# Performance work log

Measured on AMD Instinct MI355X. Metric: run time of the kernel, lower is better.

Reference implementation:

```python
import jax, jax.numpy as jnp
import numpy as np

B, C, H, W = 32, 256, 64, 64
HID = 16  # max(8, 256 // 16)


def setup_inputs() -> dict:
    key = jax.random.key(0)
    k1, k2, k3 = jax.random.split(key, 3)
    x = jax.random.normal(k1, (B, C, H, W), dtype=jnp.float32)
    # 1x1 conv weights (kernel spatial dims squeezed away)
    w1 = jax.random.normal(k2, (HID, C), dtype=jnp.float32) * (1.0 / np.sqrt(C))
    b1 = jnp.zeros((HID,), dtype=jnp.float32)
    w2 = jax.random.normal(k3, (C, HID), dtype=jnp.float32) * (1.0 / np.sqrt(HID))
    b2 = jnp.zeros((C,), dtype=jnp.float32)
    return {"x": x, "w1": w1, "b1": b1, "w2": w2, "b2": b2}


def reference(x, w1, b1, w2, b2):
    # Squeeze: global average pool over H, W -> [B, C]
    s = jnp.mean(x, axis=(2, 3))
    # Excite: two 1x1 convs on a [B,C,1,1] tensor == channel-wise MLP
    h = jax.nn.relu(jnp.einsum('bc,hc->bh', s, w1) + b1)          # [B, HID]
    g = jax.nn.sigmoid(jnp.einsum('bh,ch->bc', h, w2) + b2)       # [B, C]
    # Scale: broadcast gate over spatial dims
    return x * g[:, :, None, None]
```

## Files before the change

### kernel.cpp

```cpp
#include <hip/hip_runtime.h>
#include <math.h>

#define SE_B   32
#define SE_C   256
#define SE_HID 16
#define SE_HW  4096
#define SE_HW4 1024

__global__ __launch_bounds__(256) void se_mean_kernel(const float* __restrict__ x,
                                                      float* __restrict__ s) {
    const int plane = blockIdx.x;
    const float4* xp = (const float4*)x + (size_t)plane * SE_HW4;
    const int tid = threadIdx.x;

    float sum = 0.f;
#pragma unroll
    for (int k = 0; k < 4; ++k) {
        float4 v = xp[tid + k * 256];
        sum += (v.x + v.y) + (v.z + v.w);
    }
#pragma unroll
    for (int off = 32; off > 0; off >>= 1) sum += __shfl_down(sum, off, 64);

    __shared__ float part[4];
    if ((tid & 63) == 0) part[tid >> 6] = sum;
    __syncthreads();
    if (tid == 0) {
        float tot = (part[0] + part[1]) + (part[2] + part[3]);
        s[plane] = tot * (1.0f / SE_HW);
    }
}

__global__ __launch_bounds__(256) void se_gate_kernel(const float* __restrict__ s,
                                                      const float* __restrict__ w1,
                                                      const float* __restrict__ b1,
                                                      const float* __restrict__ w2,
                                                      const float* __restrict__ b2,
                                                      float* __restrict__ g) {
    const int b = blockIdx.x;
    const int tid = threadIdx.x;

    __shared__ float s_sh[SE_C];
    __shared__ float h_sh[SE_HID];

    s_sh[tid] = s[b * SE_C + tid];
    __syncthreads();

    if (tid < SE_HID) {
        float acc = b1[tid];
        const float* w1r = w1 + tid * SE_C;
        for (int c = 0; c < SE_C; ++c) acc = fmaf(s_sh[c], w1r[c], acc);
        h_sh[tid] = fmaxf(acc, 0.f);
    }
    __syncthreads();

    float acc = b2[tid];
    const float* w2r = w2 + tid * SE_HID;
#pragma unroll
    for (int h = 0; h < SE_HID; ++h) acc = fmaf(h_sh[h], w2r[h], acc);
    g[b * SE_C + tid] = 1.0f / (1.0f + expf(-acc));
}

__global__ __launch_bounds__(256) void se_scale_kernel(const float* __restrict__ x,
                                                       const float* __restrict__ g,
                                                       float* __restrict__ out) {
    const int total4 = SE_B * SE_C * SE_HW4;
    const float4* xp = (const float4*)x;
    float4* op = (float4*)out;
    const int stride = gridDim.x * blockDim.x;
    for (int idx = blockIdx.x * blockDim.x + threadIdx.x; idx < total4; idx += stride) {
        const float gv = g[idx >> 10];
        float4 v = xp[idx];
        v.x *= gv; v.y *= gv; v.z *= gv; v.w *= gv;
        op[idx] = v;
    }
}

extern "C" void kernel_launch(void* const* d_in, const int* in_sizes, int n_in,
                              void* d_out, int out_size, void* d_ws, size_t ws_size,
                              hipStream_t stream) {
    const float* x  = (const float*)d_in[0];
    const float* w1 = (const float*)d_in[1];
    const float* b1 = (const float*)d_in[2];
    const float* w2 = (const float*)d_in[3];
    const float* b2 = (const float*)d_in[4];
    float* out = (float*)d_out;

    float* s = (float*)d_ws;
    float* g = s + SE_B * SE_C;

    se_mean_kernel<<<SE_B * SE_C, 256, 0, stream>>>(x, s);
    se_gate_kernel<<<SE_B, 256, 0, stream>>>(s, w1, b1, w2, b2, g);
    se_scale_kernel<<<8192, 256, 0, stream>>>(x, g, out);
}
```

Measured before the change: 256.3 us.

## Fuse gate MLP into per-plane scale kernel with nontemporal stores

Removes the separate gate kernel. Each scale block, one per (b,c) plane, now recomputes the tiny excitation MLP for its batch from the pooled means and applies the gate directly. The x loads are issued before the gate computation to overlap latency, and outputs are written with nontemporal stores to avoid polluting cache. This saves one kernel launch and the global round trip for g, at the cost of redundant MLP work per block and extra syncthreads.

```diff
diff --git a/kernel.cpp b/kernel.cpp
--- a/kernel.cpp
+++ b/kernel.cpp
@@ -6,6 +6,8 @@
 #define SE_HID 16
 #define SE_HW  4096
 #define SE_HW4 1024
+
+typedef float f4v __attribute__((ext_vector_type(4)));
 
 __global__ __launch_bounds__(256) void se_mean_kernel(const float* __restrict__ x,
                                                       float* __restrict__ s) {
@@ -31,49 +33,66 @@
     }
 }
 
-__global__ __launch_bounds__(256) void se_gate_kernel(const float* __restrict__ s,
-                                                      const float* __restrict__ w1,
-                                                      const float* __restrict__ b1,
-                                                      const float* __restrict__ w2,
-                                                      const float* __restrict__ b2,
-                                                      float* __restrict__ g) {
-    const int b = blockIdx.x;
+__global__ __launch_bounds__(256) void se_scale_kernel(const float* __restrict__ x,
+                                                       const float* __restrict__ s,
+                                                       const float* __restrict__ w1,
+                                                       const float* __restrict__ b1,
+                                                       const float* __restrict__ w2,
+                                                       const float* __restrict__ b2,
+                                                       float* __restrict__ out) {
+    const int plane = blockIdx.x;
+    const int b = plane >> 8;
+    const int c = plane & 255;
     const int tid = threadIdx.x;
 
-    __shared__ float s_sh[SE_C];
-    __shared__ float h_sh[SE_HID];
+    const float4* xp = (const float4*)x + (size_t)plane * SE_HW4;
+    float4* op = (float4*)out + (size_t)plane * SE_HW4;
 
-    s_sh[tid] = s[b * SE_C + tid];
+    float4 v0 = xp[tid];
+    float4 v1 = xp[tid + 256];
+    float4 v2 = xp[tid + 512];
+    float4 v3 = xp[tid + 768];
+
+    __shared__ float part[16][17];
+    __shared__ float g_sh;
+
+    const int i = tid & 15;
+    const int j = tid >> 4;
+    {
+        const float* srow = s  + b * SE_C  + j * 16;
+        const float* wrow = w1 + i * SE_C  + j * 16;
+        float p = 0.f;
+#pragma unroll
+        for (int k = 0; k < 16; ++k) p = fmaf(srow[k], wrow[k], p);
+        part[j][i] = p;
+    }
     __syncthreads();
-
     if (tid < SE_HID) {
         float acc = b1[tid];
-        const float* w1r = w1 + tid * SE_C;
-        for (int c = 0; c < SE_C; ++c) acc = fmaf(s_sh[c], w1r[c], acc);
-        h_sh[tid] = fmaxf(acc, 0.f);
+#pragma unroll
+        for (int k = 0; k < 16; ++k) acc += part[k][tid];
+        part[0][tid] = fmaxf(acc, 0.f);
     }
     __syncthreads();
+    if (tid == 0) {
+        float acc = b2[c];
+        const float* w2r = w2 + c * SE_HID;
+#pragma unroll
+        for (int k = 0; k < 16; ++k) acc = fmaf(part[0][k], w2r[k], acc);
+        g_sh = 1.0f / (1.0f + expf(-acc));
+    }
+    __syncthreads();
+    const float g = g_sh;
 
-    float acc = b2[tid];
-    const float* w2r = w2 + tid * SE_HID;
-#pragma unroll
-    for (int h = 0; h < SE_HID; ++h) acc = fmaf(h_sh[h], w2r[h], acc);
-    g[b * SE_C + tid] = 1.0f / (1.0f + expf(-acc));
-}
+    v0.x *= g; v0.y *= g; v0.z *= g; v0.w *= g;
+    v1.x *= g; v1.y *= g; v1.z *= g; v1.w *= g;
+    v2.x *= g; v2.y *= g; v2.z *= g; v2.w *= g;
+    v3.x *= g; v3.y *= g; v3.z *= g; v3.w *= g;
 
-__global__ __launch_bounds__(256) void se_scale_kernel(const float* __restrict__ x,
-                                                       const float* __restrict__ g,
-                                                       float* __restrict__ out) {
-    const int total4 = SE_B * SE_C * SE_HW4;
-    const float4* xp = (const float4*)x;
-    float4* op = (float4*)out;
-    const int stride = gridDim.x * blockDim.x;
-    for (int idx = blockIdx.x * blockDim.x + threadIdx.x; idx < total4; idx += stride) {
-        const float gv = g[idx >> 10];
-        float4 v = xp[idx];
-        v.x *= gv; v.y *= gv; v.z *= gv; v.w *= gv;
-        op[idx] = v;
-    }
+    __builtin_nontemporal_store(*(f4v*)&v0, (f4v*)(op + tid));
+    __builtin_nontemporal_store(*(f4v*)&v1, (f4v*)(op + tid + 256));
+    __builtin_nontemporal_store(*(f4v*)&v2, (f4v*)(op + tid + 512));
+    __builtin_nontemporal_store(*(f4v*)&v3, (f4v*)(op + tid + 768));
 }
 
 extern "C" void kernel_launch(void* const* d_in, const int* in_sizes, int n_in,
@@ -87,9 +106,7 @@
     float* out = (float*)d_out;
 
     float* s = (float*)d_ws;
-    float* g = s + SE_B * SE_C;
 
     se_mean_kernel<<<SE_B * SE_C, 256, 0, stream>>>(x, s);
-    se_gate_kernel<<<SE_B, 256, 0, stream>>>(s, w1, b1, w2, b2, g);
-    se_scale_kernel<<<8192, 256, 0, stream>>>(x, g, out);
+    se_scale_kernel<<<SE_B * SE_C, 256, 0, stream>>>(x, s, w1, b1, w2, b2, out);
 }
```

After: 249.9 us. 1.03x faster.

## Fuse gate MLP into mean kernel via last-block atomic; per-plane scale with nontemporal stores

Applied to the files above, without the earlier changes.

The mean reduction now counts finished blocks with an atomic counter, and the last block computes the whole excitation MLP for all batches. This replaces the separate gate kernel, at the cost of a tiny init kernel that resets the counter. The scale kernel is restructured to one block per plane, so the gate is loaded once per block instead of per element, and it writes output with nontemporal stores to avoid polluting the cache. The MLP now runs on a single block, and the serial tail of that last block adds latency.

```diff
diff --git a/kernel.cpp b/kernel.cpp
--- a/kernel.cpp
+++ b/kernel.cpp
@@ -6,12 +6,21 @@
 #define SE_HID 16
 #define SE_HW  4096
 #define SE_HW4 1024
+#define SE_PLANES (SE_B * SE_C)
 
-__global__ __launch_bounds__(256) void se_mean_kernel(const float* __restrict__ x,
-                                                      float* __restrict__ s) {
+typedef float f4v __attribute__((ext_vector_type(4)));
+
+__global__ void se_init_kernel(unsigned int* counter) { *counter = 0u; }
+
+__global__ __launch_bounds__(256) void se_mean_gate_kernel(
+    const float* __restrict__ x,
+    const float* __restrict__ w1, const float* __restrict__ b1,
+    const float* __restrict__ w2, const float* __restrict__ b2,
+    float* __restrict__ s, float* __restrict__ g,
+    unsigned int* __restrict__ counter) {
     const int plane = blockIdx.x;
+    const int tid = threadIdx.x;
     const float4* xp = (const float4*)x + (size_t)plane * SE_HW4;
-    const int tid = threadIdx.x;
 
     float sum = 0.f;
 #pragma unroll
@@ -23,56 +32,60 @@
     for (int off = 32; off > 0; off >>= 1) sum += __shfl_down(sum, off, 64);
 
     __shared__ float part[4];
+    __shared__ int last_flag;
     if ((tid & 63) == 0) part[tid >> 6] = sum;
     __syncthreads();
     if (tid == 0) {
-        float tot = (part[0] + part[1]) + (part[2] + part[3]);
-        s[plane] = tot * (1.0f / SE_HW);
+        s[plane] = ((part[0] + part[1]) + (part[2] + part[3])) * (1.0f / SE_HW);
+        __threadfence();
+        unsigned int n = atomicAdd(counter, 1u);
+        last_flag = (n == SE_PLANES - 1);
     }
-}
+    __syncthreads();
+    if (!last_flag) return;
 
-__global__ __launch_bounds__(256) void se_gate_kernel(const float* __restrict__ s,
-                                                      const float* __restrict__ w1,
-                                                      const float* __restrict__ b1,
-                                                      const float* __restrict__ w2,
-                                                      const float* __restrict__ b2,
-                                                      float* __restrict__ g) {
-    const int b = blockIdx.x;
-    const int tid = threadIdx.x;
+    __threadfence();
 
-    __shared__ float s_sh[SE_C];
-    __shared__ float h_sh[SE_HID];
-
-    s_sh[tid] = s[b * SE_C + tid];
-    __syncthreads();
-
-    if (tid < SE_HID) {
-        float acc = b1[tid];
-        const float* w1r = w1 + tid * SE_C;
-        for (int c = 0; c < SE_C; ++c) acc = fmaf(s_sh[c], w1r[c], acc);
-        h_sh[tid] = fmaxf(acc, 0.f);
+    __shared__ float h_sh[SE_B][SE_HID];
+#pragma unroll
+    for (int rb = 0; rb < 2; ++rb) {
+        const int b = rb * 16 + (tid >> 4);
+        const int i = tid & 15;
+        const float* srow = s + b * SE_C;
+        const float* wrow = w1 + i * SE_C;
+        float acc = b1[i];
+        for (int c2 = 0; c2 < SE_C; ++c2) acc = fmaf(srow[c2], wrow[c2], acc);
+        h_sh[b][i] = fmaxf(acc, 0.f);
     }
     __syncthreads();
 
-    float acc = b2[tid];
-    const float* w2r = w2 + tid * SE_HID;
+    const int c = tid;
+    float wl[SE_HID];
+    const float* w2r = w2 + c * SE_HID;
 #pragma unroll
-    for (int h = 0; h < SE_HID; ++h) acc = fmaf(h_sh[h], w2r[h], acc);
-    g[b * SE_C + tid] = 1.0f / (1.0f + expf(-acc));
+    for (int k = 0; k < SE_HID; ++k) wl[k] = w2r[k];
+    const float bias = b2[c];
+    for (int b = 0; b < SE_B; ++b) {
+        float acc = bias;
+#pragma unroll
+        for (int k = 0; k < SE_HID; ++k) acc = fmaf(h_sh[b][k], wl[k], acc);
+        g[b * SE_C + c] = 1.0f / (1.0f + expf(-acc));
+    }
 }
 
 __global__ __launch_bounds__(256) void se_scale_kernel(const float* __restrict__ x,
                                                        const float* __restrict__ g,
                                                        float* __restrict__ out) {
-    const int total4 = SE_B * SE_C * SE_HW4;
-    const float4* xp = (const float4*)x;
-    float4* op = (float4*)out;
-    const int stride = gridDim.x * blockDim.x;
-    for (int idx = blockIdx.x * blockDim.x + threadIdx.x; idx < total4; idx += stride) {
-        const float gv = g[idx >> 10];
-        float4 v = xp[idx];
+    const int plane = blockIdx.x;
+    const int tid = threadIdx.x;
+    const float gv = g[plane];
+    const float4* xp = (const float4*)x + (size_t)plane * SE_HW4;
+    float4* op = (float4*)out + (size_t)plane * SE_HW4;
+#pragma unroll
+    for (int k = 0; k < 4; ++k) {
+        float4 v = xp[tid + k * 256];
         v.x *= gv; v.y *= gv; v.z *= gv; v.w *= gv;
-        op[idx] = v;
+        __builtin_nontemporal_store(*(f4v*)&v, (f4v*)(op + tid + k * 256));
     }
 }
 
@@ -86,10 +99,11 @@
     const float* b2 = (const float*)d_in[4];
     float* out = (float*)d_out;
 
-    float* s = (float*)d_ws;
-    float* g = s + SE_B * SE_C;
+    unsigned int* counter = (unsigned int*)d_ws;
+    float* s = (float*)d_ws + 16;
+    float* g = s + SE_PLANES;
 
-    se_mean_kernel<<<SE_B * SE_C, 256, 0, stream>>>(x, s);
-    se_gate_kernel<<<SE_B, 256, 0, stream>>>(s, w1, b1, w2, b2, g);
-    se_scale_kernel<<<8192, 256, 0, stream>>>(x, g, out);
+    se_init_kernel<<<1, 1, 0, stream>>>(counter);
+    se_mean_gate_kernel<<<SE_PLANES, 256, 0, stream>>>(x, w1, b1, w2, b2, s, g, counter);
+    se_scale_kernel<<<SE_PLANES, 256, 0, stream>>>(x, g, out);
 }
```

Result: slower. 600.6 us (+134.3%).
